# Performance work log

Measured on AMD Instinct MI355X. Metric: run time of the kernel, lower is better.

## Reference

```python
import jax, jax.numpy as jnp
import numpy as np

B, H, SQ, SK, D = 2, 16, 2048, 2048, 128
P_DROP = 0.5


def setup_inputs() -> dict:
    key = jax.random.key(0)
    kq, kk, kv, km = jax.random.split(key, 4)
    query = jax.random.normal(kq, (B, H, SQ, D), dtype=jnp.float32)
    key_t = jax.random.normal(kk, (B, H, SK, D), dtype=jnp.float32)
    value = jax.random.normal(kv, (B, H, SK, D), dtype=jnp.float32)
    # deterministic Bernoulli(0.5) keep-mask standing in for dropout(p=0.5, train=True)
    dropout_mask = jax.random.randint(km, (B, H, SQ, SK), 0, 2, dtype=jnp.int32)
    return {"query": query, "key": key_t, "value": value, "dropout_mask": dropout_mask}


def reference(query, key, value, dropout_mask):
    d = query.shape[-1]
    # original: scaled_qk = qk.div(d ** -0.5)  ==  qk * sqrt(d)  (faithful to source)
    scale = jnp.asarray(d, query.dtype) ** 0.5
    qk = jnp.einsum("bhqd,bhkd->bhqk", query, key)  # [B,H,SQ,SK]
    scaled_qk = qk * scale
    keep_scale = jnp.asarray(1.0 / (1.0 - P_DROP), query.dtype)
    dropped = jnp.where(dropout_mask == 1, scaled_qk * keep_scale, jnp.zeros((), query.dtype))
    out = jnp.einsum("bhqk,bhkd->bhqd", dropped, value)  # [B,H,SQ,D]
    return out
```

## Files before the change

kernel.cpp:

```cpp
#include <hip/hip_runtime.h>
#include <hip/hip_bf16.h>

#define B_   2
#define H_   16
#define SQ_  2048
#define SK_  2048
#define D_   128

#define QT   128
#define KT   32
#define NITER (SK_/KT)

using bf16x8 = __attribute__((ext_vector_type(8))) __bf16;
using bf16x4 = __attribute__((ext_vector_type(4))) __bf16;
using bf16x2 = __attribute__((ext_vector_type(2))) __bf16;
using f32x4  = __attribute__((ext_vector_type(4))) float;

#define MFMA16(a,b,c) __builtin_amdgcn_mfma_f32_16x16x32_bf16(a,b,c,0,0,0)

#define K_PITCH  136
#define VT_PITCH 40

#define KB_   (KT*K_PITCH*2)
#define VTB_  (D_*VT_PITCH*2)
#define SMEM_BYTES (2*KB_ + 2*VTB_)

__global__ __launch_bounds__(512, 4)
void attn_drop_kernel(const float* __restrict__ Q,
                      const float* __restrict__ K,
                      const float* __restrict__ V,
                      const int*   __restrict__ M,
                      float* __restrict__ Out)
{
    __shared__ __align__(16) char smem[SMEM_BYTES];

    const int tid  = threadIdx.x;
    const int wave = tid >> 6;
    const int lane = tid & 63;
    const int quad = lane >> 4;
    const int ln   = lane & 15;

    const int orig = ((blockIdx.x & 7) << 6) | (blockIdx.x >> 3);
    const int bh = orig >> 4;
    const int qb = orig & 15;

    const int kt0 = (bh * 5) & (NITER - 1);

    const float* qptr = Q + ((size_t)bh*SQ_ + (size_t)qb*QT) * D_;
    const float* kptr = K + (size_t)bh*SK_*D_;
    const float* vptr = V + (size_t)bh*SK_*D_;
    const int*   mptr = M + (size_t)bh*(size_t)SQ_*SK_ + (size_t)qb*QT*SK_;
    float*       optr = Out + ((size_t)bh*SQ_ + (size_t)qb*QT) * D_;

    const int c  = tid & 31;
    const int g  = tid >> 5;

    const int wxor = (2*g) ^ ((c & 3) * 8);

    const int* mlane = mptr + (size_t)(16*wave + ln)*SK_ + 4*quad;

    const int x3  = (ln >> 2) & 3;
    const int p0c = (quad >> 1) ^ x3;
    const int vlo = 8*p0c       + 4*(quad & 1);
    const int vhi = 8*(p0c ^ 2) + 4*(quad & 1);

    float4 kpre0, kpre1, vpre0, vpre1;

    auto load_kv = [&](int kt) {
        const float4* ks = (const float4*)(kptr + (size_t)kt*KT*D_);
        const float4* vs = (const float4*)(vptr + (size_t)kt*KT*D_);
        kpre0 = ks[g*32 + c];
        kpre1 = ks[(g+16)*32 + c];
        vpre0 = vs[(2*g  )*32 + c];
        vpre1 = vs[(2*g+1)*32 + c];
    };

    auto write_tile = [&](int b) {
        __bf16* ksb = (__bf16*)(smem + b*KB_);
        __bf16* vtb = (__bf16*)(smem + 2*KB_ + b*VTB_);
        {
            bf16x4 h0 = { (__bf16)kpre0.x, (__bf16)kpre0.y, (__bf16)kpre0.z, (__bf16)kpre0.w };
            bf16x4 h1 = { (__bf16)kpre1.x, (__bf16)kpre1.y, (__bf16)kpre1.z, (__bf16)kpre1.w };
            *(bf16x4*)&ksb[ g    *K_PITCH + 4*c] = h0;
            *(bf16x4*)&ksb[(g+16)*K_PITCH + 4*c] = h1;
        }
        {
            const float* f0 = (const float*)&vpre0;
            const float* f1 = (const float*)&vpre1;
            #pragma unroll
            for (int j = 0; j < 4; ++j) {
                bf16x2 pr = { (__bf16)f0[j], (__bf16)f1[j] };
                *(bf16x2*)&vtb[(4*c + j)*VT_PITCH + wxor] = pr;
            }
        }
    };

    load_kv(kt0);
    int4 mA0 = *(const int4*)(mlane + kt0*KT);
    int4 mA1 = *(const int4*)(mlane + kt0*KT + 16);
    int4 mB0, mB1;

    bf16x8 qf[4];
    {
        const float* qrow = qptr + (size_t)(16*wave + ln)*D_;
        #pragma unroll
        for (int s = 0; s < 4; ++s) {
            float4 a  = *(const float4*)(qrow + 32*s + 8*quad);
            float4 b2 = *(const float4*)(qrow + 32*s + 8*quad + 4);
            qf[s] = (bf16x8){ (__bf16)a.x,  (__bf16)a.y,  (__bf16)a.z,  (__bf16)a.w,
                              (__bf16)b2.x, (__bf16)b2.y, (__bf16)b2.z, (__bf16)b2.w };
        }
    }

    f32x4 Oacc[8];
    #pragma unroll
    for (int dt = 0; dt < 8; ++dt)
        Oacc[dt] = (f32x4){0.f, 0.f, 0.f, 0.f};

    const int row0 = 16*wave + 4*quad;

#define STEP(ITI, BSEL, mc0, mc1, mn0, mn1)                                          \
    {                                                                                \
        write_tile(BSEL);                                                            \
        asm volatile("s_waitcnt lgkmcnt(0)" ::: "memory");                           \
        __builtin_amdgcn_s_barrier();                                                \
        if ((ITI) + 1 < NITER) {                                                     \
            const int ktn = ((ITI) + 1 + kt0) & (NITER - 1);                         \
            load_kv(ktn);                                                            \
            mn0 = *(const int4*)(mlane + ktn*KT);                                    \
            mn1 = *(const int4*)(mlane + ktn*KT + 16);                               \
        }                                                                            \
        const __bf16* ksb = (const __bf16*)(smem + (BSEL)*KB_);                      \
        const __bf16* vtb = (const __bf16*)(smem + 2*KB_ + (BSEL)*VTB_);             \
        f32x4 S0 = (f32x4){0.f,0.f,0.f,0.f};                                         \
        f32x4 S1 = (f32x4){0.f,0.f,0.f,0.f};                                         \
        __builtin_amdgcn_s_setprio(1);                                               \
        _Pragma("unroll")                                                            \
        for (int s = 0; s < 4; ++s) {                                                \
            bf16x8 kf0 = *(const bf16x8*)&ksb[ ln    *K_PITCH + 32*s + 8*quad];      \
            bf16x8 kf1 = *(const bf16x8*)&ksb[(16+ln)*K_PITCH + 32*s + 8*quad];      \
            S0 = MFMA16(kf0, qf[s], S0);                                             \
            S1 = MFMA16(kf1, qf[s], S1);                                             \
        }                                                                            \
        __builtin_amdgcn_s_setprio(0);                                               \
        bf16x8 pa;                                                                   \
        pa[0] = mc0.x ? (__bf16)S0[0] : (__bf16)0.0f;                                \
        pa[1] = mc0.y ? (__bf16)S0[1] : (__bf16)0.0f;                                \
        pa[2] = mc0.z ? (__bf16)S0[2] : (__bf16)0.0f;                                \
        pa[3] = mc0.w ? (__bf16)S0[3] : (__bf16)0.0f;                                \
        pa[4] = mc1.x ? (__bf16)S1[0] : (__bf16)0.0f;                                \
        pa[5] = mc1.y ? (__bf16)S1[1] : (__bf16)0.0f;                                \
        pa[6] = mc1.z ? (__bf16)S1[2] : (__bf16)0.0f;                                \
        pa[7] = mc1.w ? (__bf16)S1[3] : (__bf16)0.0f;                                \
        __builtin_amdgcn_s_setprio(1);                                               \
        _Pragma("unroll")                                                            \
        for (int dt = 0; dt < 8; ++dt) {                                             \
            const __bf16* vrow = &vtb[(16*dt + ln)*VT_PITCH];                        \
            bf16x4 va = *(const bf16x4*)&vrow[vlo];                                  \
            bf16x4 vb = *(const bf16x4*)&vrow[vhi];                                  \
            bf16x8 vf = { va[0], va[1], va[2], va[3], vb[0], vb[1], vb[2], vb[3] };  \
            Oacc[dt] = MFMA16(pa, vf, Oacc[dt]);                                     \
        }                                                                            \
        __builtin_amdgcn_s_setprio(0);                                               \
    }

    for (int it = 0; it < NITER; it += 2) {
        STEP(it,     0, mA0, mA1, mB0, mB1);
        STEP(it + 1, 1, mB0, mB1, mA0, mA1);
    }
#undef STEP

    const float SCALE = 22.62741699796952f;
    #pragma unroll
    for (int dt = 0; dt < 8; ++dt) {
        #pragma unroll
        for (int r = 0; r < 4; ++r)
            optr[(size_t)(row0 + r)*D_ + 16*dt + ln] = Oacc[dt][r] * SCALE;
    }
}

extern "C" void kernel_launch(void* const* d_in, const int* in_sizes, int n_in,
                              void* d_out, int out_size, void* d_ws, size_t ws_size,
                              hipStream_t stream) {
    (void)in_sizes; (void)n_in; (void)d_ws; (void)ws_size; (void)out_size;
    const float* Q = (const float*)d_in[0];
    const float* K = (const float*)d_in[1];
    const float* V = (const float*)d_in[2];
    const int*   M = (const int*)d_in[3];
    float* Out = (float*)d_out;

    dim3 grid(B_ * H_ * (SQ_ / QT));
    attn_drop_kernel<<<grid, 512, 0, stream>>>(Q, K, V, M, Out);
}
```

Measured before the change: 781.8 us.

## Prefetch dropout mask in 256-column superstep chunks packed into bitmasks

Restructures the dropout-mask loading: each lane now loads wide contiguous runs of its mask row for a whole 8-tile superstep, packs the values into 32-bit bitmasks, and redistributes bits to the MFMA lanes with ds_bpermute. The aim is to turn many small scattered 16-byte mask loads into longer coalesced runs issued well ahead of use, improving latency hiding for the dominant mask traffic. In exchange it adds bpermute ops, packing ALU work and extra registers, and the start tile is now aligned to superstep boundaries.

```diff
diff --git a/kernel.cpp b/kernel.cpp
--- a/kernel.cpp
+++ b/kernel.cpp
@@ -10,6 +10,7 @@
 #define QT   128
 #define KT   32
 #define NITER (SK_/KT)
+#define NSS   8
 
 using bf16x8 = __attribute__((ext_vector_type(8))) __bf16;
 using bf16x4 = __attribute__((ext_vector_type(4))) __bf16;
@@ -44,7 +45,7 @@
     const int bh = orig >> 4;
     const int qb = orig & 15;
 
-    const int kt0 = (bh * 5) & (NITER - 1);
+    const int kt0 = ((bh * 5) & 7) * 8;
 
     const float* qptr = Q + ((size_t)bh*SQ_ + (size_t)qb*QT) * D_;
     const float* kptr = K + (size_t)bh*SK_*D_;
@@ -56,13 +57,13 @@
     const int g  = tid >> 5;
 
     const int wxor = (2*g) ^ ((c & 3) * 8);
-
-    const int* mlane = mptr + (size_t)(16*wave + ln)*SK_ + 4*quad;
-
     const int x3  = (ln >> 2) & 3;
     const int p0c = (quad >> 1) ^ x3;
     const int vlo = 8*p0c       + 4*(quad & 1);
     const int vhi = 8*(p0c ^ 2) + 4*(quad & 1);
+
+    const int* mrow = mptr + (size_t)(16*wave + ln)*SK_ + 64*quad;
+    const int  baddr = 4*ln;
 
     float4 kpre0, kpre1, vpre0, vpre1;
 
@@ -96,9 +97,25 @@
     };
 
     load_kv(kt0);
-    int4 mA0 = *(const int4*)(mlane + kt0*KT);
-    int4 mA1 = *(const int4*)(mlane + kt0*KT + 16);
-    int4 mB0, mB1;
+
+    unsigned mcur0, mcur1;
+    {
+        const int pb0 = kt0 * KT;
+        int4 mm[16];
+        #pragma unroll
+        for (int n = 0; n < 16; ++n) mm[n] = *(const int4*)(mrow + pb0 + 4*n);
+        unsigned w0 = 0, w1 = 0;
+        #pragma unroll
+        for (int n = 0; n < 8; ++n) {
+            unsigned na = (unsigned)(mm[n].x&1)   | ((unsigned)(mm[n].y&1)<<1)
+                        | ((unsigned)(mm[n].z&1)<<2) | ((unsigned)(mm[n].w&1)<<3);
+            unsigned nb = (unsigned)(mm[n+8].x&1)   | ((unsigned)(mm[n+8].y&1)<<1)
+                        | ((unsigned)(mm[n+8].z&1)<<2) | ((unsigned)(mm[n+8].w&1)<<3);
+            w0 |= na << (4*n);
+            w1 |= nb << (4*n);
+        }
+        mcur0 = w0; mcur1 = w1;
+    }
 
     bf16x8 qf[4];
     {
@@ -119,39 +136,65 @@
 
     const int row0 = 16*wave + 4*quad;
 
-#define STEP(ITI, BSEL, mc0, mc1, mn0, mn1)                                          \
+    unsigned mn0, mn1;
+    int4 t0b, t1b, t2b, t3b;
+
+#define ISSUE(BB)                                                                    \
+    { const int pbn = ((((kt0>>3) + s + 1) & 7) << 8) + 16*(BB);                     \
+      t0b = *(const int4*)(mrow + pbn);                                              \
+      t1b = *(const int4*)(mrow + pbn + 4);                                          \
+      t2b = *(const int4*)(mrow + pbn + 8);                                          \
+      t3b = *(const int4*)(mrow + pbn + 12); }
+
+#define PACK(BB)                                                                     \
+    { unsigned p16 =  ((unsigned)(t0b.x&1)    | ((unsigned)(t0b.y&1)<<1)             \
+                    | ((unsigned)(t0b.z&1)<<2)| ((unsigned)(t0b.w&1)<<3))            \
+                   | (((unsigned)(t1b.x&1)    | ((unsigned)(t1b.y&1)<<1)             \
+                    | ((unsigned)(t1b.z&1)<<2)| ((unsigned)(t1b.w&1)<<3)) << 4)      \
+                   | (((unsigned)(t2b.x&1)    | ((unsigned)(t2b.y&1)<<1)             \
+                    | ((unsigned)(t2b.z&1)<<2)| ((unsigned)(t2b.w&1)<<3)) << 8)      \
+                   | (((unsigned)(t3b.x&1)    | ((unsigned)(t3b.y&1)<<1)             \
+                    | ((unsigned)(t3b.z&1)<<2)| ((unsigned)(t3b.w&1)<<3)) << 12);    \
+      if ((BB) == 0) mn0 |= p16;                                                     \
+      if ((BB) == 1) mn0 |= p16 << 16;                                               \
+      if ((BB) == 2) mn1 |= p16;                                                     \
+      if ((BB) == 3) mn1 |= p16 << 16; }
+
+#define STEP(J, MASKOPS)                                                             \
     {                                                                                \
-        write_tile(BSEL);                                                            \
+        write_tile((J) & 1);                                                         \
         asm volatile("s_waitcnt lgkmcnt(0)" ::: "memory");                           \
         __builtin_amdgcn_s_barrier();                                                \
-        if ((ITI) + 1 < NITER) {                                                     \
-            const int ktn = ((ITI) + 1 + kt0) & (NITER - 1);                         \
-            load_kv(ktn);                                                            \
-            mn0 = *(const int4*)(mlane + ktn*KT);                                    \
-            mn1 = *(const int4*)(mlane + ktn*KT + 16);                               \
-        }                                                                            \
-        const __bf16* ksb = (const __bf16*)(smem + (BSEL)*KB_);                      \
-        const __bf16* vtb = (const __bf16*)(smem + 2*KB_ + (BSEL)*VTB_);             \
+        { const int itn = 8*s + (J) + 1;                                             \
+          if (itn < NITER) load_kv((itn + kt0) & (NITER - 1)); }                     \
+        MASKOPS                                                                      \
+        const __bf16* ksb = (const __bf16*)(smem + ((J)&1)*KB_);                     \
+        const __bf16* vtb = (const __bf16*)(smem + 2*KB_ + ((J)&1)*VTB_);            \
         f32x4 S0 = (f32x4){0.f,0.f,0.f,0.f};                                         \
         f32x4 S1 = (f32x4){0.f,0.f,0.f,0.f};                                         \
         __builtin_amdgcn_s_setprio(1);                                               \
         _Pragma("unroll")                                                            \
-        for (int s = 0; s < 4; ++s) {                                                \
-            bf16x8 kf0 = *(const bf16x8*)&ksb[ ln    *K_PITCH + 32*s + 8*quad];      \
-            bf16x8 kf1 = *(const bf16x8*)&ksb[(16+ln)*K_PITCH + 32*s + 8*quad];      \
-            S0 = MFMA16(kf0, qf[s], S0);                                             \
-            S1 = MFMA16(kf1, qf[s], S1);                                             \
+        for (int ss = 0; ss < 4; ++ss) {                                             \
+            bf16x8 kf0 = *(const bf16x8*)&ksb[ ln    *K_PITCH + 32*ss + 8*quad];     \
+            bf16x8 kf1 = *(const bf16x8*)&ksb[(16+ln)*K_PITCH + 32*ss + 8*quad];     \
+            S0 = MFMA16(kf0, qf[ss], S0);                                            \
+            S1 = MFMA16(kf1, qf[ss], S1);                                            \
         }                                                                            \
         __builtin_amdgcn_s_setprio(0);                                               \
+                \
+        unsigned wd = (unsigned)__builtin_amdgcn_ds_bpermute(                        \
+            baddr + 64*((J) >> 1), (int)(((J) & 1) ? mcur1 : mcur0));                \
+        unsigned lo = wd >> (4*quad);                                                \
+        unsigned hi = wd >> (16 + 4*quad);                                           \
         bf16x8 pa;                                                                   \
-        pa[0] = mc0.x ? (__bf16)S0[0] : (__bf16)0.0f;                                \
-        pa[1] = mc0.y ? (__bf16)S0[1] : (__bf16)0.0f;                                \
-        pa[2] = mc0.z ? (__bf16)S0[2] : (__bf16)0.0f;                                \
-        pa[3] = mc0.w ? (__bf16)S0[3] : (__bf16)0.0f;                                \
-        pa[4] = mc1.x ? (__bf16)S1[0] : (__bf16)0.0f;                                \
-        pa[5] = mc1.y ? (__bf16)S1[1] : (__bf16)0.0f;                                \
-        pa[6] = mc1.z ? (__bf16)S1[2] : (__bf16)0.0f;                                \
-        pa[7] = mc1.w ? (__bf16)S1[3] : (__bf16)0.0f;                                \
+        pa[0] = (lo & 1u) ? (__bf16)S0[0] : (__bf16)0.0f;                            \
+        pa[1] = (lo & 2u) ? (__bf16)S0[1] : (__bf16)0.0f;                            \
+        pa[2] = (lo & 4u) ? (__bf16)S0[2] : (__bf16)0.0f;                            \
+        pa[3] = (lo & 8u) ? (__bf16)S0[3] : (__bf16)0.0f;                            \
+        pa[4] = (hi & 1u) ? (__bf16)S1[0] : (__bf16)0.0f;                            \
+        pa[5] = (hi & 2u) ? (__bf16)S1[1] : (__bf16)0.0f;                            \
+        pa[6] = (hi & 4u) ? (__bf16)S1[2] : (__bf16)0.0f;                            \
+        pa[7] = (hi & 8u) ? (__bf16)S1[3] : (__bf16)0.0f;                            \
         __builtin_amdgcn_s_setprio(1);                                               \
         _Pragma("unroll")                                                            \
         for (int dt = 0; dt < 8; ++dt) {                                             \
@@ -164,11 +207,23 @@
         __builtin_amdgcn_s_setprio(0);                                               \
     }
 
-    for (int it = 0; it < NITER; it += 2) {
-        STEP(it,     0, mA0, mA1, mB0, mB1);
-        STEP(it + 1, 1, mB0, mB1, mA0, mA1);
+    for (int s = 0; s < NSS; ++s) {
+        const bool more = (s + 1 < NSS);
+        mn0 = 0; mn1 = 0;
+        STEP(0, { if (more) ISSUE(0); })
+        STEP(1, {})
+        STEP(2, { if (more) { PACK(0); ISSUE(1); } })
+        STEP(3, {})
+        STEP(4, { if (more) { PACK(1); ISSUE(2); } })
+        STEP(5, {})
+        STEP(6, { if (more) { PACK(2); ISSUE(3); } })
+        STEP(7, {})
+        if (more) PACK(3);
+        mcur0 = mn0; mcur1 = mn1;
     }
 #undef STEP
+#undef ISSUE
+#undef PACK
 
     const float SCALE = 22.62741699796952f;
     #pragma unroll
```

New measurement: 991.7 us. 26.8% more time.
